# Performance work log

Hardware: AMD Instinct MI355X
Metric: run time of the kernel (lower is better)

The kernel has to match this reference:

```python
import jax, jax.numpy as jnp
import numpy as np

B, C, H, W = 4, 64, 512, 512
NS = 2048   # n_samples edges per image
NL = 1000   # number of superpixel labels


def setup_inputs() -> dict:
    key = jax.random.key(0)
    k1, k2, k3, k4 = jax.random.split(key, 4)
    x = jax.random.normal(k1, (B, C, H, W), dtype=jnp.float32)
    label_maps = jax.random.randint(k2, (B, 1, H, W), 0, NL).astype(jnp.int32)
    edges = jax.random.randint(k3, (B, NS, 2), 0, NL).astype(jnp.int32)
    edge_weights = (jax.random.uniform(k4, (B, NS)) > 0.5).astype(jnp.float32)
    return {"x": x, "label_maps": label_maps, "edges": edges,
            "edge_weights": edge_weights, "n_labels": NL}


def reference(x, label_maps, edges, edge_weights, n_labels):
    # x: [B,C,H,W]; label_maps: [B,1,H,W] int; edges: [B,NS,2] int; edge_weights: [B,NS]
    Bd, Cd, Hd, Wd = x.shape

    def per_image_means(xi, li):
        feats = xi.reshape(Cd, Hd * Wd).T            # [HW, C]
        lab = li.reshape(-1)                          # [HW]
        sums = jax.ops.segment_sum(feats, lab, num_segments=n_labels)   # [NL, C]
        cnts = jax.ops.segment_sum(jnp.ones((Hd * Wd,), xi.dtype), lab,
                                   num_segments=n_labels)               # [NL]
        return sums / jnp.maximum(cnts, 1)[:, None]

    means = jax.vmap(per_image_means)(x, label_maps[:, 0])  # [B, NL, C]

    bi = jnp.arange(Bd)[:, None]                  # [B,1] batch index
    xa = means[bi, edges[..., 0]]                 # [B, NS, C] mean feats at edge endpoint 0
    xb = means[bi, edges[..., 1]]                 # [B, NS, C] mean feats at edge endpoint 1
    y = edge_weights[..., None]                   # [B, NS, 1] edge weight labels
    return xa, xb, y
```

## Files before the change

### kernel.cpp

```cpp
#include <hip/hip_runtime.h>

#define Bd 4
#define Cd 64
#define HWp 262144
#define NSd 2048
#define NLd 1000

#define NWIN   256
#define PXW    4096
#define NSL    16
#define CSL    4
#define SPB    8
#define PU32   2000

typedef float __attribute__((ext_vector_type(4))) floatx4;

#define OFF_PART  0
#define OFF_BCNT  (NWIN * NSL * PU32)
#define OFF_MEANS (OFF_BCNT + NWIN * NLd)
#define WS_ELEMS  (OFF_MEANS + Bd * NLd * Cd)

__device__ __forceinline__ unsigned short f2bf(float f) {
    unsigned u = __float_as_uint(f);
    u += 0x7FFFu + ((u >> 16) & 1u);
    return (unsigned short)(u >> 16);
}
__device__ __forceinline__ unsigned pack2(float lo, float hi) {
    return ((unsigned)f2bf(hi) << 16) | (unsigned)f2bf(lo);
}
__device__ __forceinline__ float bflo(unsigned u) { return __uint_as_float(u << 16); }
__device__ __forceinline__ float bfhi(unsigned u) { return __uint_as_float(u & 0xFFFF0000u); }
__device__ __forceinline__ int clampl(int l) {
    return (l < 0) ? 0 : (l >= NLd ? NLd - 1 : l);
}

__global__ __launch_bounds__(1024, 8)
void fused_kernel(const float* __restrict__ x, const int* __restrict__ lab,
                  int* __restrict__ blockCnt, unsigned* __restrict__ partial) {
    __shared__ int h[1024];
    __shared__ uint2 ordered[PXW];

    const int tid  = threadIdx.x;
    const int half = blockIdx.x;
    const int w    = blockIdx.y;
    const int b    = w >> 6;
    const int p0   = (w & 63) * PXW;

    h[tid] = 0;
    __syncthreads();

    const int4 lv = ((const int4*)(lab + ((size_t)b << 18) + p0))[tid];
    const int l0 = clampl(lv.x), l1 = clampl(lv.y),
              l2 = clampl(lv.z), l3 = clampl(lv.w);
    atomicAdd(&h[l0], 1);
    atomicAdd(&h[l1], 1);
    atomicAdd(&h[l2], 1);
    atomicAdd(&h[l3], 1);
    __syncthreads();

    const int myCnt = h[tid];
    if (half == 0 && tid < NLd) blockCnt[(size_t)w * NLd + tid] = myCnt;
    for (int off = 1; off < 1024; off <<= 1) {
        int t = (tid >= off) ? h[tid - off] : 0;
        __syncthreads();
        h[tid] += t;
        __syncthreads();
    }
    const int myst = h[tid] - myCnt;
    __syncthreads();
    h[tid] = myst;
    __syncthreads();

    const int r0 = atomicAdd(&h[l0], 1) & (PXW - 1);
    const int r1 = atomicAdd(&h[l1], 1) & (PXW - 1);
    const int r2 = atomicAdd(&h[l2], 1) & (PXW - 1);
    const int r3 = atomicAdd(&h[l3], 1) & (PXW - 1);

    const float* __restrict__ xs =
        x + (((size_t)b * Cd + half * (SPB * CSL)) << 18) + p0 + 4 * tid;
    unsigned* __restrict__ pout =
        partial + ((size_t)w * NSL + half * SPB) * PU32;

    floatx4 v0, v1, v2, v3;
    v0 = __builtin_nontemporal_load((const floatx4*)(xs + ((size_t)0 << 18)));
    v1 = __builtin_nontemporal_load((const floatx4*)(xs + ((size_t)1 << 18)));
    v2 = __builtin_nontemporal_load((const floatx4*)(xs + ((size_t)2 << 18)));
    v3 = __builtin_nontemporal_load((const floatx4*)(xs + ((size_t)3 << 18)));
    uint2 pk0, pk1, pk2, pk3;
    pk0.x = pack2(v0[0], v1[0]); pk0.y = pack2(v2[0], v3[0]);
    pk1.x = pack2(v0[1], v1[1]); pk1.y = pack2(v2[1], v3[1]);
    pk2.x = pack2(v0[2], v1[2]); pk2.y = pack2(v2[2], v3[2]);
    pk3.x = pack2(v0[3], v1[3]); pk3.y = pack2(v2[3], v3[3]);

    for (int s = 0; s < SPB; ++s) {
        __syncthreads();
        ordered[r0] = pk0;
        ordered[r1] = pk1;
        ordered[r2] = pk2;
        ordered[r3] = pk3;
        if (s + 1 < SPB) {
            const float* nb = xs + (((size_t)((s + 1) * CSL)) << 18);
            v0 = __builtin_nontemporal_load((const floatx4*)(nb + ((size_t)0 << 18)));
            v1 = __builtin_nontemporal_load((const floatx4*)(nb + ((size_t)1 << 18)));
            v2 = __builtin_nontemporal_load((const floatx4*)(nb + ((size_t)2 << 18)));
            v3 = __builtin_nontemporal_load((const floatx4*)(nb + ((size_t)3 << 18)));
        }
        __syncthreads();

        if (tid < NLd) {
            float a0 = 0, a1 = 0, a2 = 0, a3 = 0;
            for (int i = 0; i < myCnt; ++i) {
                uint2 u = ordered[(myst + i) & (PXW - 1)];
                a0 += bflo(u.x); a1 += bfhi(u.x);
                a2 += bflo(u.y); a3 += bfhi(u.y);
            }
            uint2 o; o.x = pack2(a0, a1); o.y = pack2(a2, a3);
            *(uint2*)(pout + (size_t)s * PU32 + tid * 2) = o;
        }
        if (s + 1 < SPB) {
            pk0.x = pack2(v0[0], v1[0]); pk0.y = pack2(v2[0], v3[0]);
            pk1.x = pack2(v0[1], v1[1]); pk1.y = pack2(v2[1], v3[1]);
            pk2.x = pack2(v0[2], v1[2]); pk2.y = pack2(v2[2], v3[2]);
            pk3.x = pack2(v0[3], v1[3]); pk3.y = pack2(v2[3], v3[3]);
        }
    }
}

__global__ __launch_bounds__(256)
void combine_kernel(const unsigned* __restrict__ partial,
                    const int* __restrict__ blockCnt,
                    float* __restrict__ means) {
    __shared__ float ninv[16];
    const int tid = threadIdx.x;
    const int b   = blockIdx.y;
    const int l0  = blockIdx.x * 16;
    const int s   = tid >> 4;
    const int ll  = tid & 15;
    const int l   = l0 + ll;

    if (tid < 16) {
        const int li = (l0 + tid < NLd) ? (l0 + tid) : (NLd - 1);
        int n = 0;
        for (int g = 0; g < 64; ++g)
            n += blockCnt[(size_t)(b * 64 + g) * NLd + li];
        ninv[tid] = 1.0f / (float)(n > 0 ? n : 1);
    }
    __syncthreads();

    if (l < NLd) {
        float r0 = 0, r1 = 0, r2 = 0, r3 = 0;
        const unsigned* __restrict__ pb =
            partial + ((size_t)(b * 64) * NSL + s) * PU32 + l * 2;
        for (int g = 0; g < 64; ++g) {
            uint2 p = *(const uint2*)(pb + (size_t)g * NSL * PU32);
            r0 += bflo(p.x); r1 += bfhi(p.x);
            r2 += bflo(p.y); r3 += bfhi(p.y);
        }
        const float sc = ninv[ll];
        float4 o; o.x = r0 * sc; o.y = r1 * sc; o.z = r2 * sc; o.w = r3 * sc;
        *(float4*)(means + (((size_t)(b * NLd + l)) << 6) + s * 4) = o;
    }
}

__global__ __launch_bounds__(256)
void gather_kernel(const float* __restrict__ means,
                   const int* __restrict__ edges,
                   const float* __restrict__ ew,
                   float* __restrict__ out) {
    const int t  = blockIdx.x * 256 + threadIdx.x;
    const int bs = t >> 6;
    const int c  = t & 63;
    const int b  = bs >> 11;

    const int la = clampl(edges[bs * 2 + 0]);
    const int lb = clampl(edges[bs * 2 + 1]);

    out[t] = means[((size_t)(b * NLd + la) << 6) + c];
    out[(size_t)Bd * NSd * Cd + t] = means[((size_t)(b * NLd + lb) << 6) + c];
    if (t < Bd * NSd)
        out[2 * (size_t)Bd * NSd * Cd + t] = ew[t];
}

#define WS_FB_ELEMS (Bd * Cd * NLd + Bd * NLd)

__global__ __launch_bounds__(256)
void fb_sums_kernel(const float* __restrict__ x, const int* __restrict__ lab,
                    float* __restrict__ sums) {
    __shared__ float lsum[NLd];
    const int tid   = threadIdx.x;
    const int chunk = blockIdx.x;
    const int c     = blockIdx.y;
    const int b     = blockIdx.z;

    for (int l = tid; l < NLd; l += 256) lsum[l] = 0.0f;
    __syncthreads();

    const float4* __restrict__ xp =
        (const float4*)x + (size_t)(b * Cd + c) * (HWp / 4);
    const int4* __restrict__ lp = (const int4*)lab + (size_t)b * (HWp / 4);

    const int nvec = HWp / 16;
    const int v0 = chunk * nvec, v1 = v0 + nvec;
    for (int v = v0 + tid; v < v1; v += 256) {
        float4 xv = xp[v];
        int4   lv = lp[v];
        atomicAdd(&lsum[clampl(lv.x)], xv.x);
        atomicAdd(&lsum[clampl(lv.y)], xv.y);
        atomicAdd(&lsum[clampl(lv.z)], xv.z);
        atomicAdd(&lsum[clampl(lv.w)], xv.w);
    }
    __syncthreads();

    float* __restrict__ dst = sums + (size_t)(b * Cd + c) * NLd;
    for (int l = tid; l < NLd; l += 256)
        atomicAdd(&dst[l], lsum[l]);
}

__global__ __launch_bounds__(256)
void fb_counts_kernel(const int* __restrict__ lab, float* __restrict__ counts) {
    __shared__ unsigned lcnt[NLd];
    const int tid   = threadIdx.x;
    const int chunk = blockIdx.x;
    const int b     = blockIdx.y;

    for (int l = tid; l < NLd; l += 256) lcnt[l] = 0u;
    __syncthreads();

    const int4* __restrict__ lp = (const int4*)lab + (size_t)b * (HWp / 4);
    const int nvec = HWp / 16;
    const int v0 = chunk * nvec, v1 = v0 + nvec;
    for (int v = v0 + tid; v < v1; v += 256) {
        int4 lv = lp[v];
        atomicAdd(&lcnt[clampl(lv.x)], 1u);
        atomicAdd(&lcnt[clampl(lv.y)], 1u);
        atomicAdd(&lcnt[clampl(lv.z)], 1u);
        atomicAdd(&lcnt[clampl(lv.w)], 1u);
    }
    __syncthreads();

    float* __restrict__ dst = counts + (size_t)b * NLd;
    for (int l = tid; l < NLd; l += 256)
        atomicAdd(&dst[l], (float)lcnt[l]);
}

__global__ __launch_bounds__(256)
void fb_gather_kernel(const float* __restrict__ sums,
                      const float* __restrict__ counts,
                      const int* __restrict__ edges,
                      const float* __restrict__ ew,
                      float* __restrict__ out) {
    const int t  = blockIdx.x * 256 + threadIdx.x;
    const int bs = t >> 6;
    const int c  = t & 63;
    const int b  = bs >> 11;

    const int la = clampl(edges[bs * 2 + 0]);
    const int lb = clampl(edges[bs * 2 + 1]);

    const float ca = fmaxf(counts[b * NLd + la], 1.0f);
    const float cb = fmaxf(counts[b * NLd + lb], 1.0f);

    const size_t plane = (size_t)(b * Cd + c) * NLd;
    out[t] = sums[plane + la] / ca;
    out[(size_t)Bd * NSd * Cd + t] = sums[plane + lb] / cb;
    if (t < Bd * NSd)
        out[2 * (size_t)Bd * NSd * Cd + t] = ew[t];
}

extern "C" void kernel_launch(void* const* d_in, const int* in_sizes, int n_in,
                              void* d_out, int out_size, void* d_ws, size_t ws_size,
                              hipStream_t stream) {
    const float* x     = (const float*)d_in[0];
    const int*   lab   = (const int*)d_in[1];
    const int*   edges = (const int*)d_in[2];
    const float* ew    = (const float*)d_in[3];
    float*       out   = (float*)d_out;

    const int n_gather = Bd * NSd * Cd;

    if (ws_size >= (size_t)WS_ELEMS * sizeof(float)) {
        unsigned* partial  = (unsigned*)d_ws + OFF_PART;
        int*      blockCnt = (int*)d_ws + OFF_BCNT;
        float*    means    = (float*)d_ws + OFF_MEANS;

        fused_kernel<<<dim3(2, NWIN), 1024, 0, stream>>>(x, lab, blockCnt, partial);
        combine_kernel<<<dim3(63, Bd), 256, 0, stream>>>(partial, blockCnt, means);
        gather_kernel<<<n_gather / 256, 256, 0, stream>>>(means, edges, ew, out);
    } else {
        float* sums   = (float*)d_ws;
        float* counts = sums + (size_t)Bd * Cd * NLd;

        hipMemsetAsync(d_ws, 0, (size_t)WS_FB_ELEMS * sizeof(float), stream);

        fb_sums_kernel<<<dim3(4, Cd, Bd), 256, 0, stream>>>(x, lab, sums);
        fb_counts_kernel<<<dim3(4, Bd), 256, 0, stream>>>(lab, counts);
        fb_gather_kernel<<<n_gather / 256, 256, 0, stream>>>(sums, counts, edges, ew, out);
    }
}
```

Measured before the change: 78.44 us.

## Split label histogram and ranking into separate kernel ahead of feature reduction

Moves the per-window label histogram, prefix scan and per-pixel rank computation out of the fused feature kernel into a new rank_kernel that writes counts, start offsets and ranks to workspace. The fused kernel then reads these precomputed values instead of redoing the histogram and scan in each of its two channel-half blocks. This removes duplicated shared-memory atomics and scan barriers and frees shared memory in the main kernel, at the cost of an extra launch and an extra global write and read of the rank array.

```diff
diff --git a/kernel.cpp b/kernel.cpp
--- a/kernel.cpp
+++ b/kernel.cpp
@@ -17,7 +17,9 @@
 
 #define OFF_PART  0
 #define OFF_BCNT  (NWIN * NSL * PU32)
-#define OFF_MEANS (OFF_BCNT + NWIN * NLd)
+#define OFF_BST   (OFF_BCNT + NWIN * NLd)
+#define OFF_RANK  (OFF_BST + NWIN * NLd)
+#define OFF_MEANS (OFF_RANK + NWIN * PXW)
 #define WS_ELEMS  (OFF_MEANS + Bd * NLd * Cd)
 
 __device__ __forceinline__ unsigned short f2bf(float f) {
@@ -34,17 +36,14 @@
     return (l < 0) ? 0 : (l >= NLd ? NLd - 1 : l);
 }
 
-__global__ __launch_bounds__(1024, 8)
-void fused_kernel(const float* __restrict__ x, const int* __restrict__ lab,
-                  int* __restrict__ blockCnt, unsigned* __restrict__ partial) {
+__global__ __launch_bounds__(1024)
+void rank_kernel(const int* __restrict__ lab, int* __restrict__ blockCnt,
+                 int* __restrict__ blockSt, int* __restrict__ rank) {
     __shared__ int h[1024];
-    __shared__ uint2 ordered[PXW];
-
-    const int tid  = threadIdx.x;
-    const int half = blockIdx.x;
-    const int w    = blockIdx.y;
-    const int b    = w >> 6;
-    const int p0   = (w & 63) * PXW;
+    const int tid = threadIdx.x;
+    const int w   = blockIdx.x;
+    const int b   = w >> 6;
+    const int p0  = (w & 63) * PXW;
 
     h[tid] = 0;
     __syncthreads();
@@ -59,7 +58,7 @@
     __syncthreads();
 
     const int myCnt = h[tid];
-    if (half == 0 && tid < NLd) blockCnt[(size_t)w * NLd + tid] = myCnt;
+    if (tid < NLd) blockCnt[(size_t)w * NLd + tid] = myCnt;
     for (int off = 1; off < 1024; off <<= 1) {
         int t = (tid >= off) ? h[tid - off] : 0;
         __syncthreads();
@@ -67,14 +66,43 @@
         __syncthreads();
     }
     const int myst = h[tid] - myCnt;
+    if (tid < NLd) blockSt[(size_t)w * NLd + tid] = myst;
     __syncthreads();
     h[tid] = myst;
     __syncthreads();
 
-    const int r0 = atomicAdd(&h[l0], 1) & (PXW - 1);
-    const int r1 = atomicAdd(&h[l1], 1) & (PXW - 1);
-    const int r2 = atomicAdd(&h[l2], 1) & (PXW - 1);
-    const int r3 = atomicAdd(&h[l3], 1) & (PXW - 1);
+    int4 rv;
+    rv.x = atomicAdd(&h[l0], 1) & (PXW - 1);
+    rv.y = atomicAdd(&h[l1], 1) & (PXW - 1);
+    rv.z = atomicAdd(&h[l2], 1) & (PXW - 1);
+    rv.w = atomicAdd(&h[l3], 1) & (PXW - 1);
+    ((int4*)(rank + ((size_t)w << 12)))[tid] = rv;
+}
+
+__global__ __launch_bounds__(1024, 8)
+void fused_kernel(const float* __restrict__ x, const int* __restrict__ rank,
+                  const int* __restrict__ blockCnt, const int* __restrict__ blockSt,
+                  unsigned* __restrict__ partial) {
+    __shared__ uint2 ordered[PXW];
+
+    const int tid  = threadIdx.x;
+    const int half = blockIdx.x;
+    const int w    = blockIdx.y;
+    const int b    = w >> 6;
+    const int p0   = (w & 63) * PXW;
+
+    int4 rv = ((const int4*)(rank + ((size_t)w << 12)))[tid];
+    const int r0 = rv.x & (PXW - 1), r1 = rv.y & (PXW - 1),
+              r2 = rv.z & (PXW - 1), r3 = rv.w & (PXW - 1);
+
+    int myCnt = 0, myst = 0;
+    if (tid < NLd) {
+        myCnt = blockCnt[(size_t)w * NLd + tid];
+        myst  = blockSt [(size_t)w * NLd + tid];
+        if (myst < 0) myst = 0; if (myst > PXW) myst = PXW;
+        if (myCnt < 0) myCnt = 0;
+        if (myCnt > PXW - myst) myCnt = PXW - myst;
+    }
 
     const float* __restrict__ xs =
         x + (((size_t)b * Cd + half * (SPB * CSL)) << 18) + p0 + 4 * tid;
@@ -281,9 +309,12 @@
     if (ws_size >= (size_t)WS_ELEMS * sizeof(float)) {
         unsigned* partial  = (unsigned*)d_ws + OFF_PART;
         int*      blockCnt = (int*)d_ws + OFF_BCNT;
+        int*      blockSt  = (int*)d_ws + OFF_BST;
+        int*      rank     = (int*)d_ws + OFF_RANK;
         float*    means    = (float*)d_ws + OFF_MEANS;
 
-        fused_kernel<<<dim3(2, NWIN), 1024, 0, stream>>>(x, lab, blockCnt, partial);
+        rank_kernel<<<NWIN, 1024, 0, stream>>>(lab, blockCnt, blockSt, rank);
+        fused_kernel<<<dim3(2, NWIN), 1024, 0, stream>>>(x, rank, blockCnt, blockSt, partial);
         combine_kernel<<<dim3(63, Bd), 256, 0, stream>>>(partial, blockCnt, means);
         gather_kernel<<<n_gather / 256, 256, 0, stream>>>(means, edges, ew, out);
     } else {
```

After: 81.87 us. 1.04x slower.
